# Kernel tuning notes

Measured on AMD Instinct MI355X. Metric: run time of the kernel, lower is better.

## Reference

```python
import jax, jax.numpy as jnp
import numpy as np

LEAKY_SLOPE = 0.2  # self.alpha


def setup_inputs() -> dict:
    key = jax.random.key(0)
    k1, k2, k3 = jax.random.split(key, 3)
    E, F, R = 512, 256, 4
    h = jax.random.normal(k1, (E, F), dtype=jnp.float32)
    adj = jax.random.uniform(k2, (R, E, E), dtype=jnp.float32)
    lin_w = jax.random.normal(k3, (F,), dtype=jnp.float32) * (1.0 / np.sqrt(F))
    lin_b = jnp.zeros((1,), dtype=jnp.float32)
    return {"h": h, "adj": adj, "lin_w": lin_w, "lin_b": lin_b}


def reference(h, adj, lin_w, lin_b):
    # h: [E, F], adj: [R, E, E]
    adj_agg = jax.nn.softmax(jnp.sum(adj, axis=0), axis=1)          # [E, E]
    # pairwise elementwise product: a_input[i, j] = h_i * h_j
    a_input = h[:, None, :] * h[None, :, :]                          # [E, E, F]
    attention = jax.nn.leaky_relu(adj_agg[:, :, None] * a_input,
                                  negative_slope=LEAKY_SLOPE)        # [E, E, F]
    attention = jax.nn.softmax(attention, axis=0)                    # softmax over i
    # dropout p=0.0 / eval mode -> identity
    # Linear(F -> 1): scores[i, j] = attention[i, j] . w + b
    scores = jnp.einsum('ijf,f->ij', attention, lin_w) + lin_b[0]    # [E, E]
    alpha = jax.nn.softmax(jnp.sum(scores, axis=0)[None, :, None], axis=1)  # [1, E, 1]
    # h_prime[i, f] = sum_j attention[i, j, f] * h[j, f]
    h_prime = jnp.einsum('ijf,jf->if', attention, h)                 # [E, F]
    return jax.nn.elu(h_prime), alpha
```

## Files before the change

kernel.cpp:

```cpp
#include <hip/hip_runtime.h>


typedef float f2 __attribute__((ext_vector_type(2)));
typedef float f4 __attribute__((ext_vector_type(4)));

#define EE 512
#define FF 256
#define RRR 4
#define LOG2E 1.44269504088896340736f
#define RPB 4
#define NT 16
#define CHL 32
#define FB 64

__global__ __launch_bounds__(256) void kA(const float* __restrict__ adj,
                                          float* __restrict__ s,
                                          float* __restrict__ out) {
    const int i = blockIdx.x;
    const int t = threadIdx.x;
    if (i == 0) {
        out[EE * FF + t]       = 1.0f / EE;
        out[EE * FF + 256 + t] = 1.0f / EE;
    }
    const float* base = adj + (size_t)i * EE;
    float t0 = 0.f, t1 = 0.f;
#pragma unroll
    for (int r = 0; r < RRR; ++r) {
        t0 += base[(size_t)r * EE * EE + t];
        t1 += base[(size_t)r * EE * EE + t + 256];
    }
    const float e0 = __expf(t0);
    const float e1 = __expf(t1);
    __shared__ float red[256];
    red[t] = e0 + e1;
    __syncthreads();
    for (int off = 128; off > 0; off >>= 1) {
        if (t < off) red[t] += red[t + off];
        __syncthreads();
    }
    const float inv = 1.0f / red[0];
    s[(size_t)i * EE + t]       = e0 * inv;
    s[(size_t)i * EE + t + 256] = e1 * inv;
}

__global__ __launch_bounds__(1024, 8) void kB(const float* __restrict__ h,
                                              const float* __restrict__ s,
                                              f2* __restrict__ hg) {
    const int tid  = threadIdx.x;
    const int fl   = tid & (FB - 1);
    const int team = tid >> 6;
    const int j0   = blockIdx.x * RPB;
    const int f    = blockIdx.y * FB + fl;
    __shared__ __align__(16) float sl[EE * RPB];
    __shared__ float ps[NT * RPB * FB];
#pragma unroll
    for (int p = 0; p < 2; ++p) {
        const int idx = tid + p * 1024;
        sl[idx] = s[(size_t)(idx >> 2) * EE + j0 + (idx & 3)];
    }
    __syncthreads();
    float hj0 = h[(size_t)j0 * FF + f] * LOG2E;
    float hj1 = h[(size_t)(j0 + 1) * FF + f] * LOG2E;
    float hj2 = h[(size_t)(j0 + 2) * FF + f] * LOG2E;
    float hj3 = h[(size_t)(j0 + 3) * FF + f] * LOG2E;
    float Z0 = 0.f, Z1 = 0.f, Z2 = 0.f, Z3 = 0.f;
    const float* hp = h + (size_t)(team * CHL) * FF + f;
    const f4* spv = (const f4*)(sl + team * CHL * RPB);
#pragma unroll 4
    for (int ii = 0; ii < CHL; ++ii) {
        const float hif = hp[(size_t)ii * FF];
        const f4 sv = spv[ii];
        const float y0 = sv.x * hj0 * hif;
        const float y1 = sv.y * hj1 * hif;
        const float y2 = sv.z * hj2 * hif;
        const float y3 = sv.w * hj3 * hif;
        Z0 += __builtin_amdgcn_exp2f(fmaxf(y0, 0.2f * y0));
        Z1 += __builtin_amdgcn_exp2f(fmaxf(y1, 0.2f * y1));
        Z2 += __builtin_amdgcn_exp2f(fmaxf(y2, 0.2f * y2));
        Z3 += __builtin_amdgcn_exp2f(fmaxf(y3, 0.2f * y3));
    }
    ps[(team * RPB + 0) * FB + fl] = Z0;
    ps[(team * RPB + 1) * FB + fl] = Z1;
    ps[(team * RPB + 2) * FB + fl] = Z2;
    ps[(team * RPB + 3) * FB + fl] = Z3;
    __syncthreads();
    if (tid < RPB * FB) {
        const int r = tid >> 6, fl2 = tid & (FB - 1);
        float Zt = 0.f;
#pragma unroll
        for (int t = 0; t < NT; ++t) Zt += ps[(t * RPB + r) * FB + fl2];
        const size_t o = (size_t)(j0 + r) * FF + blockIdx.y * FB + fl2;
        const float hv = h[o];
        hg[o] = (f2){hv, hv * __builtin_amdgcn_rcpf(Zt)};
    }
}

__global__ __launch_bounds__(1024, 8) void kC(const float* __restrict__ h,
                                              const float* __restrict__ s,
                                              const f2* __restrict__ hg,
                                              float* __restrict__ out) {
    const int tid  = threadIdx.x;
    const int fl   = tid & (FB - 1);
    const int team = tid >> 6;
    const int i0   = blockIdx.x * RPB;
    const int f    = blockIdx.y * FB + fl;
    __shared__ __align__(16) float sl[EE * RPB];
    __shared__ float ps[NT * RPB * FB];
#pragma unroll
    for (int p = 0; p < 2; ++p) {
        const int idx = tid + p * 1024;
        sl[idx] = s[(size_t)(i0 + (idx & 3)) * EE + (idx >> 2)];
    }
    __syncthreads();
    float hl0 = h[(size_t)i0 * FF + f] * LOG2E;
    float hl1 = h[(size_t)(i0 + 1) * FF + f] * LOG2E;
    float hl2 = h[(size_t)(i0 + 2) * FF + f] * LOG2E;
    float hl3 = h[(size_t)(i0 + 3) * FF + f] * LOG2E;
    float a0 = 0.f, a1 = 0.f, a2 = 0.f, a3 = 0.f;
    const f2* hgp = hg + (size_t)(team * CHL) * FF + f;
    const f4* spv = (const f4*)(sl + team * CHL * RPB);
#pragma unroll 4
    for (int jj = 0; jj < CHL; ++jj) {
        const f2 hgv = hgp[(size_t)jj * FF];
        const f4 sv = spv[jj];
        const float y0 = sv.x * hl0 * hgv.x;
        const float y1 = sv.y * hl1 * hgv.x;
        const float y2 = sv.z * hl2 * hgv.x;
        const float y3 = sv.w * hl3 * hgv.x;
        a0 = fmaf(__builtin_amdgcn_exp2f(fmaxf(y0, 0.2f * y0)), hgv.y, a0);
        a1 = fmaf(__builtin_amdgcn_exp2f(fmaxf(y1, 0.2f * y1)), hgv.y, a1);
        a2 = fmaf(__builtin_amdgcn_exp2f(fmaxf(y2, 0.2f * y2)), hgv.y, a2);
        a3 = fmaf(__builtin_amdgcn_exp2f(fmaxf(y3, 0.2f * y3)), hgv.y, a3);
    }
    ps[(team * RPB + 0) * FB + fl] = a0;
    ps[(team * RPB + 1) * FB + fl] = a1;
    ps[(team * RPB + 2) * FB + fl] = a2;
    ps[(team * RPB + 3) * FB + fl] = a3;
    __syncthreads();
    if (tid < RPB * FB) {
        const int r = tid >> 6, fl2 = tid & (FB - 1);
        float a = 0.f;
#pragma unroll
        for (int t = 0; t < NT; ++t) a += ps[(t * RPB + r) * FB + fl2];
        out[(size_t)(i0 + r) * FF + blockIdx.y * FB + fl2] =
            (a > 0.f) ? a : (__expf(a) - 1.0f);
    }
}

extern "C" void kernel_launch(void* const* d_in, const int* in_sizes, int n_in,
                              void* d_out, int out_size, void* d_ws, size_t ws_size,
                              hipStream_t stream) {
    const float* h   = (const float*)d_in[0];
    const float* adj = (const float*)d_in[1];

    float* s   = (float*)d_ws;
    f2*    hg  = (f2*)(s + (size_t)EE * EE);
    float* out = (float*)d_out;

    kA<<<EE, 256, 0, stream>>>(adj, s, out);
    kB<<<dim3(EE / RPB, FF / FB), 1024, 0, stream>>>(h, s, hg);
    kC<<<dim3(EE / RPB, FF / FB), 1024, 0, stream>>>(h, s, hg, out);
}
```

Before: 37.42 us.

## Retile kB/kC to 8 rows per block and 32-wide feature slices

Each block now handles 8 output rows instead of 4, with 32 teams of 32 feature lanes over chunks of 16. This reuses each loaded h/g value across 8 rows, halving global loads per exp. The interleaved (h, h/Z) float2 buffer is replaced by a single g = h/Z array, and kC reads h directly. The grid shape changes to 64x8 blocks, and there are more register accumulators per thread, which could affect occupancy.

```diff
diff --git a/kernel.cpp b/kernel.cpp
--- a/kernel.cpp
+++ b/kernel.cpp
@@ -1,17 +1,16 @@
 #include <hip/hip_runtime.h>
 
 
-typedef float f2 __attribute__((ext_vector_type(2)));
 typedef float f4 __attribute__((ext_vector_type(4)));
 
 #define EE 512
 #define FF 256
 #define RRR 4
 #define LOG2E 1.44269504088896340736f
-#define RPB 4
-#define NT 16
-#define CHL 32
-#define FB 64
+#define RPB 8
+#define NT 32
+#define CH 16
+#define FB 32
 
 __global__ __launch_bounds__(256) void kA(const float* __restrict__ adj,
                                           float* __restrict__ s,
@@ -45,104 +44,101 @@
 
 __global__ __launch_bounds__(1024, 8) void kB(const float* __restrict__ h,
                                               const float* __restrict__ s,
-                                              f2* __restrict__ hg) {
+                                              float* __restrict__ g) {
     const int tid  = threadIdx.x;
     const int fl   = tid & (FB - 1);
-    const int team = tid >> 6;
+    const int team = tid >> 5;
     const int j0   = blockIdx.x * RPB;
     const int f    = blockIdx.y * FB + fl;
     __shared__ __align__(16) float sl[EE * RPB];
     __shared__ float ps[NT * RPB * FB];
 #pragma unroll
-    for (int p = 0; p < 2; ++p) {
+    for (int p = 0; p < 4; ++p) {
         const int idx = tid + p * 1024;
-        sl[idx] = s[(size_t)(idx >> 2) * EE + j0 + (idx & 3)];
+        sl[idx] = s[(size_t)(idx >> 3) * EE + j0 + (idx & 7)];
     }
     __syncthreads();
-    float hj0 = h[(size_t)j0 * FF + f] * LOG2E;
-    float hj1 = h[(size_t)(j0 + 1) * FF + f] * LOG2E;
-    float hj2 = h[(size_t)(j0 + 2) * FF + f] * LOG2E;
-    float hj3 = h[(size_t)(j0 + 3) * FF + f] * LOG2E;
-    float Z0 = 0.f, Z1 = 0.f, Z2 = 0.f, Z3 = 0.f;
-    const float* hp = h + (size_t)(team * CHL) * FF + f;
-    const f4* spv = (const f4*)(sl + team * CHL * RPB);
+    float hj[RPB], Z[RPB];
+#pragma unroll
+    for (int r = 0; r < RPB; ++r) {
+        hj[r] = h[(size_t)(j0 + r) * FF + f] * LOG2E;
+        Z[r] = 0.f;
+    }
+    const float* hp = h + (size_t)(team * CH) * FF + f;
+    const f4* spv = (const f4*)(sl + team * CH * RPB);
 #pragma unroll 4
-    for (int ii = 0; ii < CHL; ++ii) {
+    for (int ii = 0; ii < CH; ++ii) {
         const float hif = hp[(size_t)ii * FF];
-        const f4 sv = spv[ii];
-        const float y0 = sv.x * hj0 * hif;
-        const float y1 = sv.y * hj1 * hif;
-        const float y2 = sv.z * hj2 * hif;
-        const float y3 = sv.w * hj3 * hif;
-        Z0 += __builtin_amdgcn_exp2f(fmaxf(y0, 0.2f * y0));
-        Z1 += __builtin_amdgcn_exp2f(fmaxf(y1, 0.2f * y1));
-        Z2 += __builtin_amdgcn_exp2f(fmaxf(y2, 0.2f * y2));
-        Z3 += __builtin_amdgcn_exp2f(fmaxf(y3, 0.2f * y3));
+        const f4 sa = spv[ii * 2];
+        const f4 sb = spv[ii * 2 + 1];
+        const float sv[RPB] = {sa.x, sa.y, sa.z, sa.w, sb.x, sb.y, sb.z, sb.w};
+#pragma unroll
+        for (int r = 0; r < RPB; ++r) {
+            const float y = sv[r] * hj[r] * hif;
+            Z[r] += __builtin_amdgcn_exp2f(fmaxf(y, 0.2f * y));
+        }
     }
-    ps[(team * RPB + 0) * FB + fl] = Z0;
-    ps[(team * RPB + 1) * FB + fl] = Z1;
-    ps[(team * RPB + 2) * FB + fl] = Z2;
-    ps[(team * RPB + 3) * FB + fl] = Z3;
+#pragma unroll
+    for (int r = 0; r < RPB; ++r) ps[(team * RPB + r) * FB + fl] = Z[r];
     __syncthreads();
     if (tid < RPB * FB) {
-        const int r = tid >> 6, fl2 = tid & (FB - 1);
+        const int r = tid >> 5, fq = tid & (FB - 1);
         float Zt = 0.f;
 #pragma unroll
-        for (int t = 0; t < NT; ++t) Zt += ps[(t * RPB + r) * FB + fl2];
-        const size_t o = (size_t)(j0 + r) * FF + blockIdx.y * FB + fl2;
-        const float hv = h[o];
-        hg[o] = (f2){hv, hv * __builtin_amdgcn_rcpf(Zt)};
+        for (int t = 0; t < NT; ++t) Zt += ps[(t * RPB + r) * FB + fq];
+        const size_t o = (size_t)(j0 + r) * FF + blockIdx.y * FB + fq;
+        g[o] = h[o] * __builtin_amdgcn_rcpf(Zt);
     }
 }
 
 __global__ __launch_bounds__(1024, 8) void kC(const float* __restrict__ h,
                                               const float* __restrict__ s,
-                                              const f2* __restrict__ hg,
+                                              const float* __restrict__ g,
                                               float* __restrict__ out) {
     const int tid  = threadIdx.x;
     const int fl   = tid & (FB - 1);
-    const int team = tid >> 6;
+    const int team = tid >> 5;
     const int i0   = blockIdx.x * RPB;
     const int f    = blockIdx.y * FB + fl;
     __shared__ __align__(16) float sl[EE * RPB];
     __shared__ float ps[NT * RPB * FB];
 #pragma unroll
-    for (int p = 0; p < 2; ++p) {
+    for (int p = 0; p < 4; ++p) {
         const int idx = tid + p * 1024;
-        sl[idx] = s[(size_t)(i0 + (idx & 3)) * EE + (idx >> 2)];
+        sl[idx] = s[(size_t)(i0 + (idx & 7)) * EE + (idx >> 3)];
     }
     __syncthreads();
-    float hl0 = h[(size_t)i0 * FF + f] * LOG2E;
-    float hl1 = h[(size_t)(i0 + 1) * FF + f] * LOG2E;
-    float hl2 = h[(size_t)(i0 + 2) * FF + f] * LOG2E;
-    float hl3 = h[(size_t)(i0 + 3) * FF + f] * LOG2E;
-    float a0 = 0.f, a1 = 0.f, a2 = 0.f, a3 = 0.f;
-    const f2* hgp = hg + (size_t)(team * CHL) * FF + f;
-    const f4* spv = (const f4*)(sl + team * CHL * RPB);
+    float hl[RPB], acc[RPB];
+#pragma unroll
+    for (int r = 0; r < RPB; ++r) {
+        hl[r] = h[(size_t)(i0 + r) * FF + f] * LOG2E;
+        acc[r] = 0.f;
+    }
+    const float* hp = h + (size_t)(team * CH) * FF + f;
+    const float* gp = g + (size_t)(team * CH) * FF + f;
+    const f4* spv = (const f4*)(sl + team * CH * RPB);
 #pragma unroll 4
-    for (int jj = 0; jj < CHL; ++jj) {
-        const f2 hgv = hgp[(size_t)jj * FF];
-        const f4 sv = spv[jj];
-        const float y0 = sv.x * hl0 * hgv.x;
-        const float y1 = sv.y * hl1 * hgv.x;
-        const float y2 = sv.z * hl2 * hgv.x;
-        const float y3 = sv.w * hl3 * hgv.x;
-        a0 = fmaf(__builtin_amdgcn_exp2f(fmaxf(y0, 0.2f * y0)), hgv.y, a0);
-        a1 = fmaf(__builtin_amdgcn_exp2f(fmaxf(y1, 0.2f * y1)), hgv.y, a1);
-        a2 = fmaf(__builtin_amdgcn_exp2f(fmaxf(y2, 0.2f * y2)), hgv.y, a2);
-        a3 = fmaf(__builtin_amdgcn_exp2f(fmaxf(y3, 0.2f * y3)), hgv.y, a3);
+    for (int jj = 0; jj < CH; ++jj) {
+        const float hjf = hp[(size_t)jj * FF];
+        const float gj  = gp[(size_t)jj * FF];
+        const f4 sa = spv[jj * 2];
+        const f4 sb = spv[jj * 2 + 1];
+        const float sv[RPB] = {sa.x, sa.y, sa.z, sa.w, sb.x, sb.y, sb.z, sb.w};
+#pragma unroll
+        for (int r = 0; r < RPB; ++r) {
+            const float y = sv[r] * hl[r] * hjf;
+            acc[r] = fmaf(__builtin_amdgcn_exp2f(fmaxf(y, 0.2f * y)), gj, acc[r]);
+        }
     }
-    ps[(team * RPB + 0) * FB + fl] = a0;
-    ps[(team * RPB + 1) * FB + fl] = a1;
-    ps[(team * RPB + 2) * FB + fl] = a2;
-    ps[(team * RPB + 3) * FB + fl] = a3;
+#pragma unroll
+    for (int r = 0; r < RPB; ++r) ps[(team * RPB + r) * FB + fl] = acc[r];
     __syncthreads();
     if (tid < RPB * FB) {
-        const int r = tid >> 6, fl2 = tid & (FB - 1);
+        const int r = tid >> 5, fq = tid & (FB - 1);
         float a = 0.f;
 #pragma unroll
-        for (int t = 0; t < NT; ++t) a += ps[(t * RPB + r) * FB + fl2];
-        out[(size_t)(i0 + r) * FF + blockIdx.y * FB + fl2] =
+        for (int t = 0; t < NT; ++t) a += ps[(t * RPB + r) * FB + fq];
+        out[(size_t)(i0 + r) * FF + blockIdx.y * FB + fq] =
             (a > 0.f) ? a : (__expf(a) - 1.0f);
     }
 }
@@ -154,10 +150,10 @@
     const float* adj = (const float*)d_in[1];
 
     float* s   = (float*)d_ws;
-    f2*    hg  = (f2*)(s + (size_t)EE * EE);
+    float* g   = s + (size_t)EE * EE;
     float* out = (float*)d_out;
 
     kA<<<EE, 256, 0, stream>>>(adj, s, out);
-    kB<<<dim3(EE / RPB, FF / FB), 1024, 0, stream>>>(h, s, hg);
-    kC<<<dim3(EE / RPB, FF / FB), 1024, 0, stream>>>(h, s, hg, out);
+    kB<<<dim3(EE / RPB, FF / FB), 1024, 0, stream>>>(h, s, g);
+    kC<<<dim3(EE / RPB, FF / FB), 1024, 0, stream>>>(h, s, g, out);
 }
```

After: 39.00 us. 4.2% more time.
